# Kernel tuning notes

Measured on AMD Instinct MI355X. Metric: run time of the kernel, lower is better.

The kernel has to match this reference:

```python
import jax, jax.numpy as jnp
import numpy as np

K, D, H, R, V = 4, 1024, 2048, 1024, 2048 + 4  # n_codebooks, d_model, hidden, repr, vocab
B, T = 4, 2048
LN_EPS = 1e-5


def setup_inputs() -> dict:
    key = jax.random.key(0)
    ks = jax.random.split(key, 9)
    s = 0.02
    return {
        "x": jax.random.normal(ks[0], (B, T, D), dtype=jnp.float32),
        "ln_scale": jnp.ones((K, D), dtype=jnp.float32),
        "ln_bias": jnp.zeros((K, D), dtype=jnp.float32),
        "W1": jax.random.normal(ks[1], (K, D, H), dtype=jnp.float32) * s,
        "b1": jnp.zeros((K, H), dtype=jnp.float32),
        "W2": jax.random.normal(ks[2], (K, H, R), dtype=jnp.float32) * s,
        "b2": jnp.zeros((K, R), dtype=jnp.float32),
        "Wc": jax.random.normal(ks[3], (K, R, V), dtype=jnp.float32) * s,
        "bc": jnp.zeros((K, V), dtype=jnp.float32),
    }


def reference(x, ln_scale, ln_bias, W1, b1, W2, b2, Wc, bc):
    # Shared x goes through each head's LayerNorm -> Linear -> GELU -> Linear -> classifier.
    # LayerNorm statistics depend only on x, so compute once and apply per-head affine.
    mu = jnp.mean(x, axis=-1, keepdims=True)
    var = jnp.mean(jnp.square(x - mu), axis=-1, keepdims=True)
    xn = (x - mu) * jax.lax.rsqrt(var + LN_EPS)              # [B,T,D]
    y = xn[:, None, :, :] * ln_scale[None, :, None, :] + ln_bias[None, :, None, :]  # [B,K,T,D]
    h = jax.nn.gelu(jnp.einsum('bktd,kdh->bkth', y, W1) + b1[None, :, None, :], approximate=False)
    g = jnp.einsum('bkth,khr->bktr', h, W2) + b2[None, :, None, :]   # repr [B,K,T,R]
    logits = jnp.einsum('bktr,krv->bktv', g, Wc) + bc[None, :, None, :]  # [B,K,T,V]
    return logits
```

## Files before the change

kernel.cpp:

```cpp
#include <hip/hip_runtime.h>
#include <cstdint>

#define KH   4
#define DM   1024
#define HID  2048
#define RP   1024
#define VOC  2052
#define VPAD 2176
#define TT   2048
#define MM   8192

typedef short bf16x8 __attribute__((ext_vector_type(8)));
typedef float f32x4  __attribute__((ext_vector_type(4)));

__device__ __forceinline__ unsigned short f2bf(float f) {
  union { float f; unsigned int u; } a; a.f = f;
  unsigned int u = a.u;
  unsigned int r = (u + 0x7fffu + ((u >> 16) & 1u)) >> 16;
  return (unsigned short)r;
}

__device__ __forceinline__ float fast_gelu(float v) {
  float u = v * (0.7978845608028654f + 0.035677408136300125f * v * v);
  float e = __expf(2.0f * u);
  float r = __builtin_amdgcn_rcpf(e + 1.0f);
  return v - v * r;
}

__device__ __forceinline__ void async_cp16(const unsigned short* g, unsigned short* l) {
  __builtin_amdgcn_global_load_lds(
      (const __attribute__((address_space(1))) unsigned int*)(uintptr_t)g,
      (__attribute__((address_space(3))) unsigned int*)(uintptr_t)l,
      16, 0, 0);
}

__global__ __launch_bounds__(256) void ln_kernel(const float* __restrict__ x,
                                                 unsigned short* __restrict__ xn) {
  int row = blockIdx.x;
  int tid = threadIdx.x;
  const float4* xr = (const float4*)(x + (size_t)row * DM);
  float4 v = xr[tid];
  float s  = v.x + v.y + v.z + v.w;
  float s2 = v.x * v.x + v.y * v.y + v.z * v.z + v.w * v.w;
  for (int o = 32; o > 0; o >>= 1) {
    s  += __shfl_down(s, o);
    s2 += __shfl_down(s2, o);
  }
  __shared__ float ps[8];
  int wave = tid >> 6, lane = tid & 63;
  if (lane == 0) { ps[wave] = s; ps[wave + 4] = s2; }
  __syncthreads();
  if (tid == 0) {
    float ts  = ps[0] + ps[1] + ps[2] + ps[3];
    float ts2 = ps[4] + ps[5] + ps[6] + ps[7];
    float mean = ts * (1.0f / DM);
    float var  = ts2 * (1.0f / DM) - mean * mean;
    ps[0] = mean;
    ps[1] = rsqrtf(var + 1e-5f);
  }
  __syncthreads();
  float mean = ps[0], rstd = ps[1];
  ushort4 o4;
  o4.x = f2bf((v.x - mean) * rstd);
  o4.y = f2bf((v.y - mean) * rstd);
  o4.z = f2bf((v.z - mean) * rstd);
  o4.w = f2bf((v.w - mean) * rstd);
  ((ushort4*)(xn + (size_t)row * DM))[tid] = o4;
}

__global__ __launch_bounds__(256) void fold_b1(const float* __restrict__ W1,
                                               const float* __restrict__ b1,
                                               const float* __restrict__ ln_bias,
                                               float* __restrict__ b1s) {
  int k  = blockIdx.y;
  int h0 = blockIdx.x * 64;
  int hl = threadIdx.x & 63;
  int dg = threadIdx.x >> 6;
  const float* Wk = W1 + (size_t)k * DM * HID;
  const float* lb = ln_bias + (size_t)k * DM;
  float acc = 0.f;
  for (int d = dg * 256; d < dg * 256 + 256; ++d)
    acc += lb[d] * Wk[(size_t)d * HID + h0 + hl];
  __shared__ float red[4][64];
  red[dg][hl] = acc;
  __syncthreads();
  if (dg == 0)
    b1s[(size_t)k * HID + h0 + hl] =
        b1[(size_t)k * HID + h0 + hl] + red[0][hl] + red[1][hl] + red[2][hl] + red[3][hl];
}

__global__ __launch_bounds__(256) void transpose_conv(const float* __restrict__ src,
                                                      unsigned short* __restrict__ dst,
                                                      const float* __restrict__ scale,
                                                      int Rr, int Cc, int dstHeadStride) {
  int k  = blockIdx.z;
  int c0 = blockIdx.x * 32, r0 = blockIdx.y * 32;
  int tx = threadIdx.x & 31, ty = threadIdx.x >> 5;
  __shared__ float tile[32][33];
  const float* s = src + (size_t)k * Rr * Cc;
  for (int q = 0; q < 4; q++) {
    int r = r0 + ty + q * 8;
    int c = c0 + tx;
    float v = 0.f;
    if (c < Cc) v = s[(size_t)r * Cc + c];
    if (scale) v *= scale[(size_t)k * Rr + r];
    tile[ty + q * 8][tx] = v;
  }
  __syncthreads();
  unsigned short* d = dst + (size_t)k * dstHeadStride;
  for (int q = 0; q < 4; q++) {
    int c = c0 + ty + q * 8;
    int r = r0 + tx;
    if (c < Cc) d[(size_t)c * Rr + r] = f2bf(tile[tx][ty + q * 8]);
  }
}

template <int MODE>
__global__ __launch_bounds__(256) void gemm_bt(const unsigned short* __restrict__ A,
                                               size_t aStrideH,
                                               const unsigned short* __restrict__ Bt,
                                               size_t bStrideH,
                                               const float* __restrict__ bias,
                                               int biasStrideH,
                                               unsigned short* __restrict__ ob,
                                               size_t obStrideH,
                                               float* __restrict__ of,
                                               int Kd, int ldo, int khBase) {
  __shared__ __align__(16) unsigned short As[128 * 32];
  __shared__ __align__(16) unsigned short Bs[128 * 32];

  const int kh = blockIdx.z + khBase;
  A    += (size_t)kh * aStrideH;
  Bt   += (size_t)kh * bStrideH;
  bias += (size_t)kh * biasStrideH;
  ob   += (size_t)kh * obStrideH;

  const int tile_m = blockIdx.y * 128;
  const int tile_n = blockIdx.x * 128;
  const int tid  = threadIdx.x;
  const int wave = tid >> 6;
  const int lane = tid & 63;
  const int wm = (wave & 1) * 64;
  const int wn = (wave >> 1) * 64;

  const int o0  = wave * 2048 + lane * 16;
  const int o1  = o0 + 1024;
  const int rA0 = o0 >> 6, kA0 = (o0 & 63) >> 1;
  const int rA1 = o1 >> 6, kA1 = (o1 & 63) >> 1;
  const unsigned short* gA0 = A  + (size_t)(tile_m + rA0) * Kd + kA0;
  const unsigned short* gA1 = A  + (size_t)(tile_m + rA1) * Kd + kA1;
  const unsigned short* gB0 = Bt + (size_t)(tile_n + rA0) * Kd + kA0;
  const unsigned short* gB1 = Bt + (size_t)(tile_n + rA1) * Kd + kA1;
  unsigned short* lA0 = As + wave * 1024;
  unsigned short* lA1 = As + wave * 1024 + 512;
  unsigned short* lB0 = Bs + wave * 1024;
  unsigned short* lB1 = Bs + wave * 1024 + 512;

  f32x4 acc[4][4];
#pragma unroll
  for (int i = 0; i < 4; i++)
#pragma unroll
    for (int j = 0; j < 4; j++) acc[i][j] = (f32x4){0.f, 0.f, 0.f, 0.f};

  const int al = lane & 15;
  const int kq = lane >> 4;
  const bf16x8* Ap = (const bf16x8*)As;
  const bf16x8* Bp = (const bf16x8*)Bs;

  for (int k0 = 0; k0 < Kd; k0 += 32) {
    async_cp16(gA0 + k0, lA0);
    async_cp16(gA1 + k0, lA1);
    async_cp16(gB0 + k0, lB0);
    async_cp16(gB1 + k0, lB1);
    __syncthreads();
    bf16x8 af[4], bf[4];
#pragma unroll
    for (int i = 0; i < 4; i++) af[i] = Ap[(wm + i * 16 + al) * 4 + kq];
#pragma unroll
    for (int j = 0; j < 4; j++) bf[j] = Bp[(wn + j * 16 + al) * 4 + kq];
#pragma unroll
    for (int i = 0; i < 4; i++)
#pragma unroll
      for (int j = 0; j < 4; j++)
        acc[i][j] = __builtin_amdgcn_mfma_f32_16x16x32_bf16(af[i], bf[j], acc[i][j], 0, 0, 0);
    __syncthreads();
  }

  const int rg = (lane >> 4) * 4;
#pragma unroll
  for (int j = 0; j < 4; j++) {
    int gcol = tile_n + wn + j * 16 + al;
    float bj = 0.f;
    if (MODE != 2 || gcol < VOC) bj = bias[gcol];
#pragma unroll
    for (int i = 0; i < 4; i++) {
      int grow = tile_m + wm + i * 16 + rg;
#pragma unroll
      for (int r = 0; r < 4; r++) {
        float v = acc[i][j][r] + bj;
        if (MODE == 0) {
          ob[(size_t)(grow + r) * ldo + gcol] = f2bf(fast_gelu(v));
        } else if (MODE == 1) {
          ob[(size_t)(grow + r) * ldo + gcol] = f2bf(v);
        } else {
          if (gcol < VOC) {
            int m = grow + r;
            int b = m >> 11, t = m & 2047;
            of[((size_t)(b * KH + kh) * TT + t) * VOC + gcol] = v;
          }
        }
      }
    }
  }
}

extern "C" void kernel_launch(void* const* d_in, const int* in_sizes, int n_in,
                              void* d_out, int out_size, void* d_ws, size_t ws_size,
                              hipStream_t stream) {
  const float* x        = (const float*)d_in[0];
  const float* ln_scale = (const float*)d_in[1];
  const float* ln_bias  = (const float*)d_in[2];
  const float* W1       = (const float*)d_in[3];
  const float* b1       = (const float*)d_in[4];
  const float* W2       = (const float*)d_in[5];
  const float* b2       = (const float*)d_in[6];
  const float* Wc       = (const float*)d_in[7];
  const float* bc       = (const float*)d_in[8];
  float* out = (float*)d_out;

  char* p = (char*)d_ws;
  auto alloc = [&](size_t bytes) {
    char* r = p;
    p += (bytes + 255) & ~(size_t)255;
    return r;
  };
  unsigned short* xn  = (unsigned short*)alloc((size_t)MM * DM * 2);
  unsigned short* w1t = (unsigned short*)alloc((size_t)KH * HID * DM * 2);
  float*          b1s = (float*)alloc((size_t)KH * HID * 4);
  unsigned short* w2t = (unsigned short*)alloc((size_t)KH * RP * HID * 2);
  unsigned short* wct = (unsigned short*)alloc((size_t)KH * VPAD * RP * 2);

  const size_t fixed = (size_t)(p - (char*)d_ws);
  const size_t needBatched = fixed + ((size_t)KH * MM * HID * 2 + 256) + ((size_t)KH * MM * RP * 2 + 256);
  const bool batched = ws_size >= needBatched;

  unsigned short* hbuf;
  unsigned short* gbuf;
  size_t hStride, gStride;
  if (batched) {
    hbuf = (unsigned short*)alloc((size_t)KH * MM * HID * 2);
    gbuf = (unsigned short*)alloc((size_t)KH * MM * RP * 2);
    hStride = (size_t)MM * HID;
    gStride = (size_t)MM * RP;
  } else {
    hbuf = (unsigned short*)alloc((size_t)MM * HID * 2);
    gbuf = (unsigned short*)alloc((size_t)MM * RP * 2);
    hStride = 0;
    gStride = 0;
  }

  ln_kernel<<<MM, 256, 0, stream>>>(x, xn);
  fold_b1<<<dim3(HID / 64, KH), 256, 0, stream>>>(W1, b1, ln_bias, b1s);
  transpose_conv<<<dim3(HID / 32, DM / 32, KH), 256, 0, stream>>>(W1, w1t, ln_scale, DM, HID, HID * DM);
  transpose_conv<<<dim3(RP / 32, HID / 32, KH), 256, 0, stream>>>(W2, w2t, nullptr, HID, RP, RP * HID);
  transpose_conv<<<dim3((VOC + 31) / 32, RP / 32, KH), 256, 0, stream>>>(Wc, wct, nullptr, RP, VOC, VPAD * RP);

  if (batched) {
    gemm_bt<0><<<dim3(HID / 128, MM / 128, KH), 256, 0, stream>>>(
        xn, 0, w1t, (size_t)HID * DM, b1s, HID, hbuf, hStride, nullptr, DM, HID, 0);
    gemm_bt<1><<<dim3(RP / 128, MM / 128, KH), 256, 0, stream>>>(
        hbuf, hStride, w2t, (size_t)RP * HID, b2, RP, gbuf, gStride, nullptr, HID, RP, 0);
    gemm_bt<2><<<dim3(VPAD / 128, MM / 128, KH), 256, 0, stream>>>(
        gbuf, gStride, wct, (size_t)VPAD * RP, bc, VOC, nullptr, 0, out, RP, 0, 0);
  } else {
    for (int kh = 0; kh < KH; kh++) {
      gemm_bt<0><<<dim3(HID / 128, MM / 128, 1), 256, 0, stream>>>(
          xn, 0, w1t + (size_t)kh * HID * DM, 0, b1s + (size_t)kh * HID, 0,
          hbuf, 0, nullptr, DM, HID, kh);
      gemm_bt<1><<<dim3(RP / 128, MM / 128, 1), 256, 0, stream>>>(
          hbuf, 0, w2t + (size_t)kh * RP * HID, 0, b2 + (size_t)kh * RP, 0,
          gbuf, 0, nullptr, HID, RP, kh);
      gemm_bt<2><<<dim3(VPAD / 128, MM / 128, 1), 256, 0, stream>>>(
          gbuf, 0, wct + (size_t)kh * VPAD * RP, 0, bc + (size_t)kh * VOC, 0,
          nullptr, 0, out, RP, 0, kh);
    }
  }
}
```

Measured before the change: 1.056 ms.

## Rewrite GEMM as 256x256 tile, 8-wave, double-buffered pipelined kernel with block swizzle

Replaces the 128x128 single-buffered GEMM with a 256x256 tile computed by 512 threads. Each wave now holds 8x4 MFMA accumulators. Global-to-LDS async copies for the next K-tile are interleaved with MFMA phases using explicit barriers, vmcnt waits and setprio, so memory loads overlap compute. A block-index swizzle groups workgroups to improve L2 locality. VPAD grows to a multiple of 256 and the padded weight columns are zero-filled, at the cost of more LDS per block, more registers, and some wasted work on padding.

```diff
diff --git a/kernel.cpp b/kernel.cpp
--- a/kernel.cpp
+++ b/kernel.cpp
@@ -6,7 +6,7 @@
 #define HID  2048
 #define RP   1024
 #define VOC  2052
-#define VPAD 2176
+#define VPAD 2304
 #define TT   2048
 #define MM   8192
 
@@ -92,7 +92,8 @@
 __global__ __launch_bounds__(256) void transpose_conv(const float* __restrict__ src,
                                                       unsigned short* __restrict__ dst,
                                                       const float* __restrict__ scale,
-                                                      int Rr, int Cc, int dstHeadStride) {
+                                                      int Rr, int Cc, int Cpad,
+                                                      int dstHeadStride) {
   int k  = blockIdx.z;
   int c0 = blockIdx.x * 32, r0 = blockIdx.y * 32;
   int tx = threadIdx.x & 31, ty = threadIdx.x >> 5;
@@ -111,93 +112,183 @@
   for (int q = 0; q < 4; q++) {
     int c = c0 + ty + q * 8;
     int r = r0 + tx;
-    if (c < Cc) d[(size_t)c * Rr + r] = f2bf(tile[tx][ty + q * 8]);
-  }
-}
+    if (c < Cpad) d[(size_t)c * Rr + r] = f2bf(tile[tx][ty + q * 8]);
+  }
+}
+
+
+__device__ __forceinline__ void stage_half(const unsigned short* __restrict__ g, int ldK,
+                                           unsigned short* l, int wave, int lane) {
+#pragma unroll
+  for (int r = 0; r < 2; ++r) {
+    const int Pb  = r * 8192 + wave * 1024;
+    const int P   = Pb + lane * 16;
+    const int row = P >> 6;
+    const int cb  = P & 63;
+    async_cp16(g + (size_t)row * ldK + (cb >> 1), l + (Pb >> 1));
+  }
+}
+
+#define LDSF(buf, off) (*(const bf16x8*)((buf) + (off)))
+
+#define PH_PRE()                                      \
+  __builtin_amdgcn_s_barrier();                       \
+  asm volatile("s_waitcnt lgkmcnt(0)" ::: "memory"); \
+  __builtin_amdgcn_s_setprio(1)
+
+#define PH_POST() __builtin_amdgcn_s_setprio(0)
+
+#define MROW(mi, a, B0, B1, B2, B3)                                                   \
+  acc[mi][0] = __builtin_amdgcn_mfma_f32_16x16x32_bf16(a, B0, acc[mi][0], 0, 0, 0);   \
+  acc[mi][1] = __builtin_amdgcn_mfma_f32_16x16x32_bf16(a, B1, acc[mi][1], 0, 0, 0);   \
+  acc[mi][2] = __builtin_amdgcn_mfma_f32_16x16x32_bf16(a, B2, acc[mi][2], 0, 0, 0);   \
+  acc[mi][3] = __builtin_amdgcn_mfma_f32_16x16x32_bf16(a, B3, acc[mi][3], 0, 0, 0);
+
+#define TILE4(KT, CUR, NXT)                                                          \
+  {                                                                                  \
+    const bool st = ((KT) + 1) < nkt;                                                \
+    const int kn = ((KT) + 1) << 6;                                                  \
+    bf16x8 af0, af1, af2, af3, b00, b01, b02, b03, b10, b11, b12, b13;               \
+                                                 \
+    af0 = LDSF(As[CUR][0], aoff);                                                    \
+    af1 = LDSF(As[CUR][0], aoff + 512);                                              \
+    af2 = LDSF(As[CUR][0], aoff + 1024);                                             \
+    af3 = LDSF(As[CUR][0], aoff + 1536);                                             \
+    b00 = LDSF(Bs[CUR][0], boff);                                                    \
+    b01 = LDSF(Bs[CUR][0], boff + 512);                                              \
+    b02 = LDSF(Bs[CUR][0], boff + 1024);                                             \
+    b03 = LDSF(Bs[CUR][0], boff + 1536);                                             \
+    if (st) stage_half(gA + kn, Kd, &As[NXT][0][0], wave, lane);                     \
+    PH_PRE();                                                                        \
+    MROW(0, af0, b00, b01, b02, b03)                                                 \
+    MROW(1, af1, b00, b01, b02, b03)                                                 \
+    MROW(2, af2, b00, b01, b02, b03)                                                 \
+    MROW(3, af3, b00, b01, b02, b03)                                                 \
+    PH_POST();                                                                       \
+    __builtin_amdgcn_s_barrier();                                                    \
+                                                 \
+    af0 = LDSF(As[CUR][0], aoff + 2048);                                             \
+    af1 = LDSF(As[CUR][0], aoff + 2560);                                             \
+    af2 = LDSF(As[CUR][0], aoff + 3072);                                             \
+    af3 = LDSF(As[CUR][0], aoff + 3584);                                             \
+    if (st) stage_half(gB + kn, Kd, &Bs[NXT][0][0], wave, lane);                     \
+    PH_PRE();                                                                        \
+    MROW(4, af0, b00, b01, b02, b03)                                                 \
+    MROW(5, af1, b00, b01, b02, b03)                                                 \
+    MROW(6, af2, b00, b01, b02, b03)                                                 \
+    MROW(7, af3, b00, b01, b02, b03)                                                 \
+    PH_POST();                                                                       \
+    if (st) { asm volatile("s_waitcnt vmcnt(4)" ::: "memory"); }                     \
+    else    { asm volatile("s_waitcnt vmcnt(0)" ::: "memory"); }                     \
+    __builtin_amdgcn_s_barrier();                                                    \
+                                                 \
+    af0 = LDSF(As[CUR][1], aoff);                                                    \
+    af1 = LDSF(As[CUR][1], aoff + 512);                                              \
+    af2 = LDSF(As[CUR][1], aoff + 1024);                                             \
+    af3 = LDSF(As[CUR][1], aoff + 1536);                                             \
+    b10 = LDSF(Bs[CUR][1], boff);                                                    \
+    b11 = LDSF(Bs[CUR][1], boff + 512);                                              \
+    b12 = LDSF(Bs[CUR][1], boff + 1024);                                             \
+    b13 = LDSF(Bs[CUR][1], boff + 1536);                                             \
+    if (st) stage_half(gA + kn + 32, Kd, &As[NXT][1][0], wave, lane);                \
+    PH_PRE();                                                                        \
+    MROW(0, af0, b10, b11, b12, b13)                                                 \
+    MROW(1, af1, b10, b11, b12, b13)                                                 \
+    MROW(2, af2, b10, b11, b12, b13)                                                 \
+    MROW(3, af3, b10, b11, b12, b13)                                                 \
+    PH_POST();                                                                       \
+    __builtin_amdgcn_s_barrier();                                                    \
+                                                 \
+    af0 = LDSF(As[CUR][1], aoff + 2048);                                             \
+    af1 = LDSF(As[CUR][1], aoff + 2560);                                             \
+    af2 = LDSF(As[CUR][1], aoff + 3072);                                             \
+    af3 = LDSF(As[CUR][1], aoff + 3584);                                             \
+    if (st) stage_half(gB + kn + 32, Kd, &Bs[NXT][1][0], wave, lane);                \
+    PH_PRE();                                                                        \
+    MROW(4, af0, b10, b11, b12, b13)                                                 \
+    MROW(5, af1, b10, b11, b12, b13)                                                 \
+    MROW(6, af2, b10, b11, b12, b13)                                                 \
+    MROW(7, af3, b10, b11, b12, b13)                                                 \
+    PH_POST();                                                                       \
+    if (st) { asm volatile("s_waitcnt vmcnt(4)" ::: "memory"); }                     \
+    __builtin_amdgcn_s_barrier();                                                    \
+  }
 
 template <int MODE>
-__global__ __launch_bounds__(256) void gemm_bt(const unsigned short* __restrict__ A,
-                                               size_t aStrideH,
-                                               const unsigned short* __restrict__ Bt,
-                                               size_t bStrideH,
-                                               const float* __restrict__ bias,
-                                               int biasStrideH,
-                                               unsigned short* __restrict__ ob,
-                                               size_t obStrideH,
-                                               float* __restrict__ of,
-                                               int Kd, int ldo, int khBase) {
-  __shared__ __align__(16) unsigned short As[128 * 32];
-  __shared__ __align__(16) unsigned short Bs[128 * 32];
-
-  const int kh = blockIdx.z + khBase;
+__global__ __launch_bounds__(512, 2) void gemm_bt(const unsigned short* __restrict__ A,
+                                                  size_t aStrideH,
+                                                  const unsigned short* __restrict__ Bt,
+                                                  size_t bStrideH,
+                                                  const float* __restrict__ bias,
+                                                  int biasStrideH,
+                                                  unsigned short* __restrict__ ob,
+                                                  size_t obStrideH,
+                                                  float* __restrict__ of,
+                                                  int Kd, int ldo, int khBase) {
+  __shared__ __align__(16) unsigned short As[2][2][256 * 32];
+  __shared__ __align__(16) unsigned short Bs[2][2][256 * 32];
+
+  const int X = gridDim.x, Y = gridDim.y;
+  const int lin = blockIdx.x + X * (blockIdx.y + Y * blockIdx.z);
+  const int nwg = X * Y * gridDim.z;
+  const int sw  = (lin & 7) * (nwg >> 3) + (lin >> 3);
+  const int bx  = sw % X;
+  const int t2  = sw / X;
+  const int by  = t2 % Y;
+  const int kh  = t2 / Y + khBase;
+
   A    += (size_t)kh * aStrideH;
   Bt   += (size_t)kh * bStrideH;
   bias += (size_t)kh * biasStrideH;
   ob   += (size_t)kh * obStrideH;
 
-  const int tile_m = blockIdx.y * 128;
-  const int tile_n = blockIdx.x * 128;
+  const int tile_m = by * 256;
+  const int tile_n = bx * 256;
   const int tid  = threadIdx.x;
   const int wave = tid >> 6;
   const int lane = tid & 63;
-  const int wm = (wave & 1) * 64;
-  const int wn = (wave >> 1) * 64;
-
-  const int o0  = wave * 2048 + lane * 16;
-  const int o1  = o0 + 1024;
-  const int rA0 = o0 >> 6, kA0 = (o0 & 63) >> 1;
-  const int rA1 = o1 >> 6, kA1 = (o1 & 63) >> 1;
-  const unsigned short* gA0 = A  + (size_t)(tile_m + rA0) * Kd + kA0;
-  const unsigned short* gA1 = A  + (size_t)(tile_m + rA1) * Kd + kA1;
-  const unsigned short* gB0 = Bt + (size_t)(tile_n + rA0) * Kd + kA0;
-  const unsigned short* gB1 = Bt + (size_t)(tile_n + rA1) * Kd + kA1;
-  unsigned short* lA0 = As + wave * 1024;
-  unsigned short* lA1 = As + wave * 1024 + 512;
-  unsigned short* lB0 = Bs + wave * 1024;
-  unsigned short* lB1 = Bs + wave * 1024 + 512;
-
-  f32x4 acc[4][4];
-#pragma unroll
-  for (int i = 0; i < 4; i++)
-#pragma unroll
-    for (int j = 0; j < 4; j++) acc[i][j] = (f32x4){0.f, 0.f, 0.f, 0.f};
-
+  const int wr = wave >> 2;
+  const int wc = wave & 3;
   const int al = lane & 15;
   const int kq = lane >> 4;
-  const bf16x8* Ap = (const bf16x8*)As;
-  const bf16x8* Bp = (const bf16x8*)Bs;
-
-  for (int k0 = 0; k0 < Kd; k0 += 32) {
-    async_cp16(gA0 + k0, lA0);
-    async_cp16(gA1 + k0, lA1);
-    async_cp16(gB0 + k0, lB0);
-    async_cp16(gB1 + k0, lB1);
-    __syncthreads();
-    bf16x8 af[4], bf[4];
-#pragma unroll
-    for (int i = 0; i < 4; i++) af[i] = Ap[(wm + i * 16 + al) * 4 + kq];
-#pragma unroll
-    for (int j = 0; j < 4; j++) bf[j] = Bp[(wn + j * 16 + al) * 4 + kq];
-#pragma unroll
-    for (int i = 0; i < 4; i++)
-#pragma unroll
-      for (int j = 0; j < 4; j++)
-        acc[i][j] = __builtin_amdgcn_mfma_f32_16x16x32_bf16(af[i], bf[j], acc[i][j], 0, 0, 0);
-    __syncthreads();
-  }
-
-  const int rg = (lane >> 4) * 4;
-#pragma unroll
-  for (int j = 0; j < 4; j++) {
-    int gcol = tile_n + wn + j * 16 + al;
+  const int aoff = (wr * 128 + al) * 32 + kq * 8;
+  const int boff = (wc * 64 + al) * 32 + kq * 8;
+
+  const unsigned short* gA = A  + (size_t)tile_m * Kd;
+  const unsigned short* gB = Bt + (size_t)tile_n * Kd;
+  const int nkt = Kd >> 6;
+
+  f32x4 acc[8][4];
+#pragma unroll
+  for (int i = 0; i < 8; i++)
+#pragma unroll
+    for (int j = 0; j < 4; j++) acc[i][j] = (f32x4){0.f, 0.f, 0.f, 0.f};
+
+  stage_half(gA,      Kd, &As[0][0][0], wave, lane);
+  stage_half(gB,      Kd, &Bs[0][0][0], wave, lane);
+  stage_half(gA + 32, Kd, &As[0][1][0], wave, lane);
+  stage_half(gB + 32, Kd, &Bs[0][1][0], wave, lane);
+  asm volatile("s_waitcnt vmcnt(4)" ::: "memory");
+  __builtin_amdgcn_s_barrier();
+
+#pragma unroll 1
+  for (int kt = 0; kt < nkt; kt += 2) {
+    TILE4(kt, 0, 1);
+    TILE4(kt + 1, 1, 0);
+  }
+
+  const int rg = kq * 4;
+#pragma unroll
+  for (int nj = 0; nj < 4; ++nj) {
+    const int gcol = tile_n + wc * 64 + nj * 16 + al;
     float bj = 0.f;
     if (MODE != 2 || gcol < VOC) bj = bias[gcol];
 #pragma unroll
-    for (int i = 0; i < 4; i++) {
-      int grow = tile_m + wm + i * 16 + rg;
-#pragma unroll
-      for (int r = 0; r < 4; r++) {
-        float v = acc[i][j][r] + bj;
+    for (int mi = 0; mi < 8; ++mi) {
+      const int grow = tile_m + wr * 128 + mi * 16 + rg;
+#pragma unroll
+      for (int r = 0; r < 4; ++r) {
+        float v = acc[mi][nj][r] + bj;
         if (MODE == 0) {
           ob[(size_t)(grow + r) * ldo + gcol] = f2bf(fast_gelu(v));
         } else if (MODE == 1) {
@@ -261,26 +352,26 @@
 
   ln_kernel<<<MM, 256, 0, stream>>>(x, xn);
   fold_b1<<<dim3(HID / 64, KH), 256, 0, stream>>>(W1, b1, ln_bias, b1s);
-  transpose_conv<<<dim3(HID / 32, DM / 32, KH), 256, 0, stream>>>(W1, w1t, ln_scale, DM, HID, HID * DM);
-  transpose_conv<<<dim3(RP / 32, HID / 32, KH), 256, 0, stream>>>(W2, w2t, nullptr, HID, RP, RP * HID);
-  transpose_conv<<<dim3((VOC + 31) / 32, RP / 32, KH), 256, 0, stream>>>(Wc, wct, nullptr, RP, VOC, VPAD * RP);
+  transpose_conv<<<dim3(HID / 32, DM / 32, KH), 256, 0, stream>>>(W1, w1t, ln_scale, DM, HID, HID, HID * DM);
+  transpose_conv<<<dim3(RP / 32, HID / 32, KH), 256, 0, stream>>>(W2, w2t, nullptr, HID, RP, RP, RP * HID);
+  transpose_conv<<<dim3(VPAD / 32, RP / 32, KH), 256, 0, stream>>>(Wc, wct, nullptr, RP, VOC, VPAD, VPAD * RP);
 
   if (batched) {
-    gemm_bt<0><<<dim3(HID / 128, MM / 128, KH), 256, 0, stream>>>(
+    gemm_bt<0><<<dim3(HID / 256, MM / 256, KH), 512, 0, stream>>>(
         xn, 0, w1t, (size_t)HID * DM, b1s, HID, hbuf, hStride, nullptr, DM, HID, 0);
-    gemm_bt<1><<<dim3(RP / 128, MM / 128, KH), 256, 0, stream>>>(
+    gemm_bt<1><<<dim3(RP / 256, MM / 256, KH), 512, 0, stream>>>(
         hbuf, hStride, w2t, (size_t)RP * HID, b2, RP, gbuf, gStride, nullptr, HID, RP, 0);
-    gemm_bt<2><<<dim3(VPAD / 128, MM / 128, KH), 256, 0, stream>>>(
+    gemm_bt<2><<<dim3(VPAD / 256, MM / 256, KH), 512, 0, stream>>>(
         gbuf, gStride, wct, (size_t)VPAD * RP, bc, VOC, nullptr, 0, out, RP, 0, 0);
   } else {
     for (int kh = 0; kh < KH; kh++) {
-      gemm_bt<0><<<dim3(HID / 128, MM / 128, 1), 256, 0, stream>>>(
+      gemm_bt<0><<<dim3(HID / 256, MM / 256, 1), 512, 0, stream>>>(
           xn, 0, w1t + (size_t)kh * HID * DM, 0, b1s + (size_t)kh * HID, 0,
           hbuf, 0, nullptr, DM, HID, kh);
-      gemm_bt<1><<<dim3(RP / 128, MM / 128, 1), 256, 0, stream>>>(
+      gemm_bt<1><<<dim3(RP / 256, MM / 256, 1), 512, 0, stream>>>(
           hbuf, 0, w2t + (size_t)kh * RP * HID, 0, b2 + (size_t)kh * RP, 0,
           gbuf, 0, nullptr, HID, RP, kh);
-      gemm_bt<2><<<dim3(VPAD / 128, MM / 128, 1), 256, 0, stream>>>(
+      gemm_bt<2><<<dim3(VPAD / 256, MM / 256, 1), 512, 0, stream>>>(
           gbuf, 0, wct + (size_t)kh * VPAD * RP, 0, bc + (size_t)kh * VOC, 0,
           nullptr, 0, out, RP, 0, kh);
     }
```

New measurement: 950.7 us. 10.0% less time.
